# Optimization experiments

Measured on AMD Instinct MI355X. Metric: run time of the kernel, lower is better.

Reference implementation:

```python
import jax, jax.numpy as jnp
import numpy as np

GROUP_NORM_EPS = 1e-6
NUM_GROUPS = 32


def group_norm(x, gamma, beta, num_groups=NUM_GROUPS, eps=GROUP_NORM_EPS):
    B, H, W, C = x.shape
    g = num_groups
    xg = x.reshape(B, H, W, g, C // g)
    mean = jnp.mean(xg, axis=(1, 2, 4), keepdims=True)
    var = jnp.var(xg, axis=(1, 2, 4), keepdims=True)
    xn = ((xg - mean) * jax.lax.rsqrt(var + eps)).reshape(B, H, W, C)
    return xn * gamma + beta


def setup_inputs() -> dict:
    key = jax.random.key(0)
    ks = jax.random.split(key, 6)
    B, H, W, C = 4, 64, 64, 512
    scale = 1.0 / np.sqrt(C)
    return {
        "x": jax.random.normal(ks[0], (B, H, W, C), jnp.float32),
        "gn_gamma": jnp.ones((C,), jnp.float32),
        "gn_beta": jnp.zeros((C,), jnp.float32),
        "wq": jax.random.normal(ks[1], (C, C), jnp.float32) * scale,
        "bq": jnp.zeros((C,), jnp.float32),
        "wk": jax.random.normal(ks[2], (C, C), jnp.float32) * scale,
        "bk": jnp.zeros((C,), jnp.float32),
        "wv": jax.random.normal(ks[3], (C, C), jnp.float32) * scale,
        "bv": jnp.zeros((C,), jnp.float32),
        "wo": jax.random.normal(ks[4], (C, C), jnp.float32) * scale,
        "bo": jnp.zeros((C,), jnp.float32),
    }


def reference(x, gn_gamma, gn_beta, wq, bq, wk, bk, wv, bv, wo, bo):
    B, H, W, C = x.shape
    h = group_norm(x, gn_gamma, gn_beta)
    q = h @ wq + bq  # [B,H,W,C]
    k = h @ wk + bk
    v = h @ wv + bv
    N = H * W
    qf = q.reshape(B, N, C)
    kf = k.reshape(B, N, C)
    vf = v.reshape(B, N, C)
    # full spatial self-attention: [B, N, N] score matrix
    scores = jnp.einsum('bnc,bmc->bnm', qf, kf) * (C ** -0.5)
    attn = jax.nn.softmax(scores, axis=-1)
    out = jnp.einsum('bnm,bmc->bnc', attn, vf).reshape(B, H, W, C)
    out = out @ wo + bo
    return out + x
```

## Files before the change

### kernel.cpp

```cpp
#include <hip/hip_runtime.h>

typedef __bf16 bf16x8 __attribute__((ext_vector_type(8)));
typedef float  f32x4  __attribute__((ext_vector_type(4)));
typedef float  f32x16 __attribute__((ext_vector_type(16)));
typedef unsigned long long u64x2 __attribute__((ext_vector_type(2)));
typedef unsigned short u16;
typedef unsigned short us4 __attribute__((ext_vector_type(4)));

__device__ __forceinline__ u16 f2bf(float f) {
  __bf16 h = (__bf16)f;
  return __builtin_bit_cast(u16, h);
}

__device__ __forceinline__ void gload16(const void* g, void* l) {
  __builtin_amdgcn_global_load_lds(
      (const __attribute__((address_space(1))) unsigned int*)(g),
      (__attribute__((address_space(3))) unsigned int*)(l), 16, 0, 0);
}

__device__ __forceinline__ void barrier_lgkm() {
  asm volatile("s_waitcnt lgkmcnt(0)" ::: "memory");
  __builtin_amdgcn_s_barrier();
  asm volatile("" ::: "memory");
}
template <int N> __device__ __forceinline__ void vmwait() {
  asm volatile("s_waitcnt vmcnt(%0)" :: "n"(N) : "memory");
}

__global__ void gn_partial(const float* __restrict__ x, float* __restrict__ part) {
  const int chunk = blockIdx.x, g = blockIdx.y, b = blockIdx.z;
  const int tid = threadIdx.x;
  float s = 0.f, ss = 0.f;
  const float* xb = x + ((size_t)(b * 4096 + chunk * 512)) * 512 + g * 16;
  for (int i = tid; i < 2048; i += 256) {
    const int sp = i >> 2, c4 = (i & 3) << 2;
    const float4 v = *(const float4*)(xb + (size_t)sp * 512 + c4);
    s  += v.x + v.y + v.z + v.w;
    ss += v.x * v.x + v.y * v.y + v.z * v.z + v.w * v.w;
  }
  for (int m = 32; m; m >>= 1) { s += __shfl_xor(s, m); ss += __shfl_xor(ss, m); }
  __shared__ float red[8];
  const int w = tid >> 6;
  if ((tid & 63) == 0) { red[w * 2] = s; red[w * 2 + 1] = ss; }
  __syncthreads();
  if (tid == 0) {
    float S = 0.f, SS = 0.f;
    for (int i = 0; i < 4; ++i) { S += red[2 * i]; SS += red[2 * i + 1]; }
    const int idx = ((b * 32 + g) * 8 + chunk) * 2;
    part[idx] = S; part[idx + 1] = SS;
  }
}

__global__ void gn_finalize(const float* __restrict__ part, float* __restrict__ stats) {
  const int t = threadIdx.x;
  if (t < 128) {
    float S = 0.f, SS = 0.f;
    for (int i = 0; i < 8; ++i) { S += part[(t * 8 + i) * 2]; SS += part[(t * 8 + i) * 2 + 1]; }
    const float mean = S * (1.0f / 65536.0f);
    const float var  = SS * (1.0f / 65536.0f) - mean * mean;
    stats[t * 2] = mean;
    stats[t * 2 + 1] = rsqrtf(var + 1e-6f);
  }
}

__global__ void gn_apply(const float* __restrict__ x, const float* __restrict__ gamma,
                         const float* __restrict__ beta, const float* __restrict__ stats,
                         u16* __restrict__ h) {
  const size_t i = (size_t)blockIdx.x * 256 + threadIdx.x;
  const size_t e = i * 4;
  const int c = (int)(e & 511);
  const int b = (int)(e >> 21);
  const int g = c >> 4;
  const float mean = stats[(b * 32 + g) * 2];
  const float rstd = stats[(b * 32 + g) * 2 + 1];
  const float4 xv = *(const float4*)(x + e);
  const float4 gv = *(const float4*)(gamma + c);
  const float4 bv = *(const float4*)(beta + c);
  us4 hv;
  hv.x = f2bf((xv.x - mean) * rstd * gv.x + bv.x);
  hv.y = f2bf((xv.y - mean) * rstd * gv.y + bv.y);
  hv.z = f2bf((xv.z - mean) * rstd * gv.z + bv.z);
  hv.w = f2bf((xv.w - mean) * rstd * gv.w + bv.w);
  *(us4*)(h + e) = hv;
}

__global__ void wcast_t4(const float* __restrict__ wq, const float* __restrict__ wk,
                         const float* __restrict__ wv, const float* __restrict__ wo,
                         u16* __restrict__ wT) {
  const int idx = blockIdx.x * 256 + threadIdx.x;
  const int which = idx >> 18;
  const int rr = idx & 262143;
  const float* w = (which == 0) ? wq : (which == 1) ? wk : (which == 2) ? wv : wo;
  const int n = rr >> 9, k = rr & 511;
  wT[idx] = f2bf(w[k * 512 + n]);
}

#define GEMM_STAGE(buf, t)                                                       \
  {                                                                              \
    const int k0 = (t) * 32;                                                     \
    _Pragma("unroll")                                                            \
    for (int i = 0; i < 2; ++i) {                                                \
      const int cid = tid + i * 256;                                             \
      const int row = cid >> 2, cb = cid & 3;                                    \
      const int sc = (cb ^ (row & 3)) << 3;                                      \
      gload16(A + (size_t)(brow + row) * 512 + k0 + sc, &lA[buf][cid << 3]);     \
      gload16(Bt + (size_t)(bcol0 + row) * 512 + k0 + sc, &lB[buf][cid << 3]);   \
    }                                                                            \
  }

#define GEMM_MAIN                                                                \
  const f32x4 zero4 = {0.f, 0.f, 0.f, 0.f};                                      \
  f32x4 acc[4][4];                                                               \
  _Pragma("unroll") for (int a_ = 0; a_ < 4; ++a_)                               \
  _Pragma("unroll") for (int b_ = 0; b_ < 4; ++b_) acc[a_][b_] = zero4;          \
  GEMM_STAGE(0, 0);                                                              \
  asm volatile("s_waitcnt vmcnt(0)" ::: "memory");                               \
  __syncthreads();                                                               \
  int buf = 0;                                                                   \
  for (int t = 0; t < 16; ++t) {                                                 \
    if (t < 15) GEMM_STAGE(buf ^ 1, t + 1);                                      \
    bf16x8 af[4], bfv[4];                                                        \
    _Pragma("unroll") for (int f = 0; f < 4; ++f) {                              \
      const int ra = wr * 64 + f * 16 + l15;                                     \
      af[f] = *(const bf16x8*)(&lA[buf][(ra << 5) + ((lq ^ (ra & 3)) << 3)]);    \
      const int rb = wc * 64 + f * 16 + l15;                                     \
      bfv[f] = *(const bf16x8*)(&lB[buf][(rb << 5) + ((lq ^ (rb & 3)) << 3)]);   \
    }                                                                            \
    _Pragma("unroll") for (int fa = 0; fa < 4; ++fa)                             \
    _Pragma("unroll") for (int fb = 0; fb < 4; ++fb)                             \
      acc[fa][fb] = __builtin_amdgcn_mfma_f32_16x16x32_bf16(af[fa], bfv[fb],     \
                                                            acc[fa][fb], 0, 0, 0);\
    asm volatile("s_waitcnt vmcnt(0)" ::: "memory");                             \
    __syncthreads();                                                             \
    buf ^= 1;                                                                    \
  }

__global__ __launch_bounds__(256)
void gemm_oproj(const u16* __restrict__ A, const u16* __restrict__ Bt,
                const float* __restrict__ bias, const float* __restrict__ resid,
                float* __restrict__ Cout) {
  const int tid = threadIdx.x;
  const int wid = tid >> 6, l = tid & 63;
  const int wr = wid >> 1, wc = wid & 1;
  const int l15 = l & 15, lq = l >> 4;
  const int brow = blockIdx.x * 128, bcol0 = blockIdx.y * 128;
  __shared__ u16 lA[2][4096];
  __shared__ u16 lB[2][4096];
  GEMM_MAIN
#pragma unroll
  for (int fa = 0; fa < 4; ++fa)
#pragma unroll
    for (int fb = 0; fb < 4; ++fb) {
      const int col = bcol0 + wc * 64 + fb * 16 + l15;
      const float bv = bias[col];
#pragma unroll
      for (int i = 0; i < 4; ++i) {
        const int row = brow + wr * 64 + fa * 16 + lq * 4 + i;
        const size_t idx = (size_t)row * 512 + col;
        Cout[idx] = acc[fa][fb][i] + bv + resid[idx];
      }
    }
}

__global__ __launch_bounds__(256)
void gemm_qkv(const u16* __restrict__ A, const u16* __restrict__ wT,
              const float* __restrict__ bq, const float* __restrict__ bk,
              const float* __restrict__ bv_, u16* __restrict__ q,
              u16* __restrict__ k, u16* __restrict__ v8, float qs) {
  const int tid = threadIdx.x;
  const int wid = tid >> 6, l = tid & 63;
  const int wr = wid >> 1, wc = wid & 1;
  const int l15 = l & 15, lq = l >> 4;
  const int which = blockIdx.y >> 2;
  const int brow = blockIdx.x * 128, bcol0 = (blockIdx.y & 3) * 128;
  const u16* Bt = wT + which * 262144;
  const float* bias = (which == 0) ? bq : ((which == 1) ? bk : bv_);
  __shared__ u16 lA[2][4096];
  __shared__ u16 lB[2][4096];
  GEMM_MAIN
#pragma unroll
  for (int fa = 0; fa < 4; ++fa)
#pragma unroll
    for (int fb = 0; fb < 4; ++fb) {
      const int col = bcol0 + wc * 64 + fb * 16 + l15;
      const float bb_ = bias[col];
#pragma unroll
      for (int i = 0; i < 4; ++i) {
        const int row = brow + wr * 64 + fa * 16 + lq * 4 + i;
        const float v = acc[fa][fb][i] + bb_;
        if (which == 0) {
          q[(size_t)row * 512 + col] = f2bf(v * qs);
        } else if (which == 1) {
          k[(size_t)row * 512 + col] = f2bf(v);
        } else {
          const int bb = row >> 12, n = row & 4095;
          v8[((size_t)(bb * 512 + (n >> 3))) * 4096 +
             (size_t)((col ^ ((n >> 3) & 3)) << 3) + (n & 7)] = f2bf(v);
        }
      }
    }
}

__global__ __launch_bounds__(384)
void attn_kernel(const u16* __restrict__ Q, const u16* __restrict__ K,
                 const u16* __restrict__ V8, u16* __restrict__ Oo) {
  const int bid = blockIdx.x;
  const int b = bid & 3, qb = bid >> 2;
  const int tid = threadIdx.x;
  const int wid = tid >> 6, l = tid & 63;
  const int l31 = l & 31, lh = l >> 5;

  __shared__ __align__(16) char lds[75536];
  const int PB = 65536, AB = 74752, FL = 75264, LR = 75280;

  const u16* Kb = K + (size_t)b * 2097152;
  const u16* Vb = V8 + (size_t)b * 2097152;

  const f32x16 z16 = {0.f,0.f,0.f,0.f, 0.f,0.f,0.f,0.f, 0.f,0.f,0.f,0.f, 0.f,0.f,0.f,0.f};

  if (wid < 2) {
    const int qh = wid;
    bf16x8 qf[32];
    {
      const u16* qp = Q + ((size_t)(b * 4096 + qb * 64 + qh * 32 + l31)) * 512 + lh * 8;
#pragma unroll
      for (int kk = 0; kk < 32; ++kk) qf[kk] = *(const bf16x8*)(qp + kk * 16);
    }
    barrier_lgkm();
    float m_ = -3e38f, l_ = 0.f;
    const int kxor = (l31 & 15) << 4;
    for (int t = 0; t < 128; ++t) {
      const char* kb = lds + ((t & 1) << 15) + l31 * 1024;
      f32x16 a0 = z16, a1 = z16, a2 = z16, a3 = z16;
#pragma unroll
      for (int kk = 0; kk < 32; kk += 4) {
        const bf16x8 k0 = *(const bf16x8*)(kb + ((kk * 32 + lh * 16) ^ kxor));
        a0 = __builtin_amdgcn_mfma_f32_32x32x16_bf16(k0, qf[kk], a0, 0, 0, 0);
        const bf16x8 k1 = *(const bf16x8*)(kb + (((kk + 1) * 32 + lh * 16) ^ kxor));
        a1 = __builtin_amdgcn_mfma_f32_32x32x16_bf16(k1, qf[kk + 1], a1, 0, 0, 0);
        const bf16x8 k2 = *(const bf16x8*)(kb + (((kk + 2) * 32 + lh * 16) ^ kxor));
        a2 = __builtin_amdgcn_mfma_f32_32x32x16_bf16(k2, qf[kk + 2], a2, 0, 0, 0);
        const bf16x8 k3 = *(const bf16x8*)(kb + (((kk + 3) * 32 + lh * 16) ^ kxor));
        a3 = __builtin_amdgcn_mfma_f32_32x32x16_bf16(k3, qf[kk + 3], a3, 0, 0, 0);
      }
      const f32x16 s = (a0 + a1) + (a2 + a3);
      float tmax = fmaxf(s[0], s[1]);
#pragma unroll
      for (int r2 = 2; r2 < 16; ++r2) tmax = fmaxf(tmax, s[r2]);
      tmax = fmaxf(tmax, __shfl_xor(tmax, 32));
      const bool need = tmax > m_ + 8.0f;
      const float mn = need ? tmax : m_;
      const float al = need ? __expf(m_ - mn) : 1.0f;
      float p[16];
#pragma unroll
      for (int r2 = 0; r2 < 16; ++r2) p[r2] = __expf(s[r2] - mn);
      float ps = 0.f;
#pragma unroll
      for (int r2 = 0; r2 < 16; ++r2) ps += p[r2];
      ps += __shfl_xor(ps, 32);
      l_ = l_ * al + ps;
      m_ = mn;
      char* prow = lds + PB + (t & 1) * 4608 + (qh * 32 + l31) * 72;
#pragma unroll
      for (int rg = 0; rg < 4; ++rg) {
        us4 pk4;
        pk4.x = f2bf(p[rg * 4 + 0]); pk4.y = f2bf(p[rg * 4 + 1]);
        pk4.z = f2bf(p[rg * 4 + 2]); pk4.w = f2bf(p[rg * 4 + 3]);
        *(unsigned long long*)(prow + rg * 16 + lh * 8) =
            __builtin_bit_cast(unsigned long long, pk4);
      }
      if (lh == 0) *(float*)(lds + AB + (t & 1) * 256 + (qh * 32 + l31) * 4) = al;
      const bool anyn = __any(need);
      if (l == 0) *(int*)(lds + FL + ((t & 1) * 2 + qh) * 4) = anyn ? 1 : 0;
      barrier_lgkm();
    }
    if (lh == 0) *(float*)(lds + LR + (qh * 32 + l31) * 4) = l_;
    barrier_lgkm();
  } else {
    const int dq = wid - 2;
    const int stid = (wid - 2) * 64 + l;
    {
      char* kd = lds;
#pragma unroll
      for (int i = 0; i < 8; ++i) {
        const int cid = stid + i * 256;
        const int ob = cid << 4;
        const int n_ = ob >> 10;
        const int cb = (ob & 1023) ^ ((n_ & 15) << 4);
        gload16(Kb + (size_t)n_ * 512 + (cb >> 1), kd + ob);
      }
    }
    vmwait<0>();
    barrier_lgkm();
    f32x16 o[2][4];
#pragma unroll
    for (int qt = 0; qt < 2; ++qt)
#pragma unroll
      for (int f = 0; f < 4; ++f) o[qt][f] = z16;
    bf16x8 vrA[8], vrB[8];

#define PV_APPLY(PB_, VUSE)                                                      \
    {                                                                            \
      bf16x8 pa[2][2];                                                           \
      _Pragma("unroll") for (int qt = 0; qt < 2; ++qt)                           \
      _Pragma("unroll") for (int h2 = 0; h2 < 2; ++h2) {                         \
        const char* pr = lds + PB + (PB_) * 4608 + (qt * 32 + l31) * 72 +        \
                         h2 * 32 + lh * 16;                                      \
        u64x2 w2;                                                                \
        w2[0] = *(const unsigned long long*)pr;                                  \
        w2[1] = *(const unsigned long long*)(pr + 8);                            \
        pa[qt][h2] = __builtin_bit_cast(bf16x8, w2);                             \
      }                                                                          \
      const int fl = *(const int*)(lds + FL + (PB_) * 8) |                       \
                     *(const int*)(lds + FL + (PB_) * 8 + 4);                    \
      if (fl) {                                                                  \
        _Pragma("unroll") for (int qt = 0; qt < 2; ++qt)                         \
        _Pragma("unroll") for (int rg = 0; rg < 16; ++rg) {                      \
          const int cr = (rg & 3) + 8 * (rg >> 2) + 4 * lh;                      \
          const float av = *(const float*)(lds + AB + (PB_) * 256 +              \
                                           (qt * 32 + cr) * 4);                  \
          _Pragma("unroll") for (int f = 0; f < 4; ++f) o[qt][f][rg] *= av;      \
        }                                                                        \
      }                                                                          \
      _Pragma("unroll") for (int f = 0; f < 4; ++f)                              \
      _Pragma("unroll") for (int h2 = 0; h2 < 2; ++h2) {                         \
        o[0][f] = __builtin_amdgcn_mfma_f32_32x32x16_bf16(pa[0][h2],             \
                      VUSE[f * 2 + h2], o[0][f], 0, 0, 0);                       \
        o[1][f] = __builtin_amdgcn_mfma_f32_32x32x16_bf16(pa[1][h2],             \
                      VUSE[f * 2 + h2], o[1][f], 0, 0, 0);                       \
      }                                                                          \
    }

#define PV_STEP(T, VUSE, VLOAD)                                                  \
    {                                                                            \
      const int t_ = (T);                                                        \
      if (t_ < 127) {                                                            \
        const u16* ks = Kb + (size_t)(t_ + 1) * 16384;                           \
        char* kd = lds + (((t_ + 1) & 1) << 15);                                 \
        _Pragma("unroll") for (int i = 0; i < 8; ++i) {                          \
          const int cid = stid + i * 256;                                        \
          const int ob = cid << 4;                                               \
          const int n_ = ob >> 10;                                               \
          const int cb = (ob & 1023) ^ ((n_ & 15) << 4);                         \
          gload16(ks + (size_t)n_ * 512 + (cb >> 1), kd + ob);                   \
        }                                                                        \
      }                                                                          \
      vmwait<8>();                                       \
      if (t_ > 0) { PV_APPLY((t_ - 1) & 1, VUSE) }                               \
      {                                                                          \
        const u16* vsrc = Vb + (size_t)t_ * 16384;                               \
        _Pragma("unroll") for (int f = 0; f < 4; ++f)                            \
        _Pragma("unroll") for (int h2 = 0; h2 < 2; ++h2) {                       \
          const int c4 = h2 * 2 + lh;                                            \
          const int d = dq * 128 + f * 32 + l31;                                 \
          VLOAD[f * 2 + h2] =                                                    \
              *(const bf16x8*)(vsrc + ((size_t)(c4 * 512 + (d ^ c4)) << 3));     \
        }                                                                        \
      }                                                                          \
      vmwait<8>();                              \
      barrier_lgkm();                                                            \
    }

    for (int tt = 0; tt < 64; ++tt) {
      PV_STEP(2 * tt,     vrB, vrA)
      PV_STEP(2 * tt + 1, vrA, vrB)
    }
    vmwait<0>();
    PV_APPLY(1, vrB)
    barrier_lgkm();
#undef PV_STEP
#undef PV_APPLY
#pragma unroll
    for (int qt = 0; qt < 2; ++qt)
#pragma unroll
      for (int rg = 0; rg < 16; ++rg) {
        const int cr = (rg & 3) + 8 * (rg >> 2) + 4 * lh;
        const float li = 1.0f / *(const float*)(lds + LR + (qt * 32 + cr) * 4);
        u16* orow = Oo + ((size_t)(b * 4096 + qb * 64 + qt * 32 + cr)) * 512 + dq * 128 + l31;
#pragma unroll
        for (int f = 0; f < 4; ++f) orow[f * 32] = f2bf(o[qt][f][rg] * li);
      }
  }
}

extern "C" void kernel_launch(void* const* d_in, const int* in_sizes, int n_in,
                              void* d_out, int out_size, void* d_ws, size_t ws_size,
                              hipStream_t stream) {
  const float* x     = (const float*)d_in[0];
  const float* gamma = (const float*)d_in[1];
  const float* beta  = (const float*)d_in[2];
  const float* wq    = (const float*)d_in[3];
  const float* bq    = (const float*)d_in[4];
  const float* wk    = (const float*)d_in[5];
  const float* bk    = (const float*)d_in[6];
  const float* wv    = (const float*)d_in[7];
  const float* bv    = (const float*)d_in[8];
  const float* wo    = (const float*)d_in[9];
  const float* bo    = (const float*)d_in[10];
  float* out = (float*)d_out;

  char* ws = (char*)d_ws;
  const size_t SZ = (size_t)16384 * 512;
  u16* h    = (u16*)(ws);
  u16* q    = (u16*)(ws + SZ * 2);
  u16* k    = (u16*)(ws + SZ * 4);
  u16* v8   = (u16*)(ws + SZ * 6);
  u16* aout = (u16*)(ws + SZ * 8);
  u16* wT   = (u16*)(ws + SZ * 10);
  float* part  = (float*)(ws + SZ * 10 + 4 * 262144 * 2);
  float* stats = part + 2048;

  gn_partial<<<dim3(8, 32, 4), 256, 0, stream>>>(x, part);
  gn_finalize<<<1, 128, 0, stream>>>(part, stats);
  gn_apply<<<8192, 256, 0, stream>>>(x, gamma, beta, stats, h);

  wcast_t4<<<4096, 256, 0, stream>>>(wq, wk, wv, wo, wT);

  const float qs = 0.044194173824159216f;
  gemm_qkv<<<dim3(128, 12), 256, 0, stream>>>(h, wT, bq, bk, bv, q, k, v8, qs);

  attn_kernel<<<256, 384, 0, stream>>>(q, k, v8, aout);

  gemm_oproj<<<dim3(128, 4), 256, 0, stream>>>(aout, wT + 3 * 262144, bo, x, out);
}
```

Baseline: 265.6 us.

## Split attention KV range in two and merge halves with LSE combine kernel

The attention kernel now splits each batch's 4096 keys into two halves handled by separate blocks, doubling the grid from 256 to 512 blocks so all compute units get work. Each half writes a normalized partial output plus its log-sum-exp. A new combine kernel then reweights and merges the two partial outputs, reusing the h buffer as scratch for the second half. This adds an extra pass over the output and a small bf16 rounding step at the merge. The launch bounds hint is also raised to allow more resident blocks.

```diff
diff --git a/kernel.cpp b/kernel.cpp
--- a/kernel.cpp
+++ b/kernel.cpp
@@ -201,11 +201,12 @@
     }
 }
 
-__global__ __launch_bounds__(384)
+__global__ __launch_bounds__(384, 3)
 void attn_kernel(const u16* __restrict__ Q, const u16* __restrict__ K,
-                 const u16* __restrict__ V8, u16* __restrict__ Oo) {
+                 const u16* __restrict__ V8, u16* __restrict__ Op0,
+                 u16* __restrict__ Op1, float* __restrict__ lsep) {
   const int bid = blockIdx.x;
-  const int b = bid & 3, qb = bid >> 2;
+  const int b = bid & 3, z = (bid >> 2) & 1, qb = bid >> 3;
   const int tid = threadIdx.x;
   const int wid = tid >> 6, l = tid & 63;
   const int l31 = l & 31, lh = l >> 5;
@@ -213,8 +214,8 @@
   __shared__ __align__(16) char lds[75536];
   const int PB = 65536, AB = 74752, FL = 75264, LR = 75280;
 
-  const u16* Kb = K + (size_t)b * 2097152;
-  const u16* Vb = V8 + (size_t)b * 2097152;
+  const u16* Kb = K + (size_t)b * 2097152 + (size_t)z * 1048576;
+  const u16* Vb = V8 + (size_t)b * 2097152 + (size_t)z * 1048576;
 
   const f32x16 z16 = {0.f,0.f,0.f,0.f, 0.f,0.f,0.f,0.f, 0.f,0.f,0.f,0.f, 0.f,0.f,0.f,0.f};
 
@@ -229,7 +230,7 @@
     barrier_lgkm();
     float m_ = -3e38f, l_ = 0.f;
     const int kxor = (l31 & 15) << 4;
-    for (int t = 0; t < 128; ++t) {
+    for (int t = 0; t < 64; ++t) {
       const char* kb = lds + ((t & 1) << 15) + l31 * 1024;
       f32x16 a0 = z16, a1 = z16, a2 = z16, a3 = z16;
 #pragma unroll
@@ -274,7 +275,10 @@
       if (l == 0) *(int*)(lds + FL + ((t & 1) * 2 + qh) * 4) = anyn ? 1 : 0;
       barrier_lgkm();
     }
-    if (lh == 0) *(float*)(lds + LR + (qh * 32 + l31) * 4) = l_;
+    if (lh == 0) {
+      *(float*)(lds + LR + (qh * 32 + l31) * 4) = l_;
+      lsep[z * 16384 + b * 4096 + qb * 64 + qh * 32 + l31] = m_ + __logf(l_);
+    }
     barrier_lgkm();
   } else {
     const int dq = wid - 2;
@@ -334,7 +338,7 @@
 #define PV_STEP(T, VUSE, VLOAD)                                                  \
     {                                                                            \
       const int t_ = (T);                                                        \
-      if (t_ < 127) {                                                            \
+      if (t_ < 63) {                                                             \
         const u16* ks = Kb + (size_t)(t_ + 1) * 16384;                           \
         char* kd = lds + (((t_ + 1) & 1) << 15);                                 \
         _Pragma("unroll") for (int i = 0; i < 8; ++i) {                          \
@@ -361,7 +365,7 @@
       barrier_lgkm();                                                            \
     }
 
-    for (int tt = 0; tt < 64; ++tt) {
+    for (int tt = 0; tt < 32; ++tt) {
       PV_STEP(2 * tt,     vrB, vrA)
       PV_STEP(2 * tt + 1, vrA, vrB)
     }
@@ -370,17 +374,37 @@
     barrier_lgkm();
 #undef PV_STEP
 #undef PV_APPLY
+    u16* dstb = (z == 0 ? Op0 : Op1);
 #pragma unroll
     for (int qt = 0; qt < 2; ++qt)
 #pragma unroll
       for (int rg = 0; rg < 16; ++rg) {
         const int cr = (rg & 3) + 8 * (rg >> 2) + 4 * lh;
         const float li = 1.0f / *(const float*)(lds + LR + (qt * 32 + cr) * 4);
-        u16* orow = Oo + ((size_t)(b * 4096 + qb * 64 + qt * 32 + cr)) * 512 + dq * 128 + l31;
+        u16* orow = dstb + ((size_t)(b * 4096 + qb * 64 + qt * 32 + cr)) * 512 + dq * 128 + l31;
 #pragma unroll
         for (int f = 0; f < 4; ++f) orow[f * 32] = f2bf(o[qt][f][rg] * li);
       }
   }
+}
+
+__global__ void attn_combine(u16* __restrict__ O0, const u16* __restrict__ O1,
+                             const float* __restrict__ lsep) {
+  const int idx = blockIdx.x * 256 + threadIdx.x;
+  const int row = idx >> 6;
+  const int c8 = (idx & 63) << 3;
+  const float e0 = lsep[row], e1 = lsep[16384 + row];
+  const float M = fmaxf(e0, e1);
+  float w0 = __expf(e0 - M), w1 = __expf(e1 - M);
+  const float inv = 1.0f / (w0 + w1);
+  w0 *= inv; w1 *= inv;
+  const size_t base = (size_t)row * 512 + c8;
+  const bf16x8 a = *(const bf16x8*)(O0 + base);
+  const bf16x8 c = *(const bf16x8*)(O1 + base);
+  bf16x8 rr;
+#pragma unroll
+  for (int j = 0; j < 8; ++j) rr[j] = (__bf16)(w0 * (float)a[j] + w1 * (float)c[j]);
+  *(bf16x8*)(O0 + base) = rr;
 }
 
 extern "C" void kernel_launch(void* const* d_in, const int* in_sizes, int n_in,
@@ -409,6 +433,7 @@
   u16* wT   = (u16*)(ws + SZ * 10);
   float* part  = (float*)(ws + SZ * 10 + 4 * 262144 * 2);
   float* stats = part + 2048;
+  float* lse   = stats + 256;
 
   gn_partial<<<dim3(8, 32, 4), 256, 0, stream>>>(x, part);
   gn_finalize<<<1, 128, 0, stream>>>(part, stats);
@@ -419,7 +444,8 @@
   const float qs = 0.044194173824159216f;
   gemm_qkv<<<dim3(128, 12), 256, 0, stream>>>(h, wT, bq, bk, bv, q, k, v8, qs);
 
-  attn_kernel<<<256, 384, 0, stream>>>(q, k, v8, aout);
+  attn_kernel<<<512, 384, 0, stream>>>(q, k, v8, aout, h, lse);
+  attn_combine<<<4096, 256, 0, stream>>>(aout, h, lse);
 
   gemm_oproj<<<dim3(128, 4), 256, 0, stream>>>(aout, wT + 3 * 262144, bo, x, out);
 }
```

Result: slower. 953.0 us (+258.8%).

## Double warps in attention kernel and triple-buffer K tiles

Applied to the files above, without the earlier changes.

Raises the attention block from 6 to 12 waves. Four score waves now each handle 16 query rows using 16x16x32 MFMAs, and eight PV waves each own 64 output columns. K tiles move from double to triple buffering so loads are issued two tiles ahead. The aim is more in-flight work per CU and better hiding of K load latency, at the cost of more LDS per block (about 108KB) and possibly fewer resident blocks or register pressure under the new launch bounds.

```diff
diff --git a/kernel.cpp b/kernel.cpp
--- a/kernel.cpp
+++ b/kernel.cpp
@@ -3,7 +3,6 @@
 typedef __bf16 bf16x8 __attribute__((ext_vector_type(8)));
 typedef float  f32x4  __attribute__((ext_vector_type(4)));
 typedef float  f32x16 __attribute__((ext_vector_type(16)));
-typedef unsigned long long u64x2 __attribute__((ext_vector_type(2)));
 typedef unsigned short u16;
 typedef unsigned short us4 __attribute__((ext_vector_type(4)));
 
@@ -201,7 +200,7 @@
     }
 }
 
-__global__ __launch_bounds__(384)
+__global__ __launch_bounds__(768, 3)
 void attn_kernel(const u16* __restrict__ Q, const u16* __restrict__ K,
                  const u16* __restrict__ V8, u16* __restrict__ Oo) {
   const int bid = blockIdx.x;
@@ -209,155 +208,148 @@
   const int tid = threadIdx.x;
   const int wid = tid >> 6, l = tid & 63;
   const int l31 = l & 31, lh = l >> 5;
-
-  __shared__ __align__(16) char lds[75536];
-  const int PB = 65536, AB = 74752, FL = 75264, LR = 75280;
+  const int l15 = l & 15, lq = l >> 4;
+
+  __shared__ __align__(16) char lds[108320];
+  const int PB = 98304, AB = 107520, FL = 108032, LR = 108064;
 
   const u16* Kb = K + (size_t)b * 2097152;
   const u16* Vb = V8 + (size_t)b * 2097152;
 
-  const f32x16 z16 = {0.f,0.f,0.f,0.f, 0.f,0.f,0.f,0.f, 0.f,0.f,0.f,0.f, 0.f,0.f,0.f,0.f};
-
-  if (wid < 2) {
-    const int qh = wid;
-    bf16x8 qf[32];
+  const f32x4 z4 = {0.f, 0.f, 0.f, 0.f};
+
+  if (wid < 4) {
+    const int w = wid;
+    bf16x8 qf[16];
     {
-      const u16* qp = Q + ((size_t)(b * 4096 + qb * 64 + qh * 32 + l31)) * 512 + lh * 8;
-#pragma unroll
-      for (int kk = 0; kk < 32; ++kk) qf[kk] = *(const bf16x8*)(qp + kk * 16);
+      const u16* qp = Q + ((size_t)(b * 4096 + qb * 64 + w * 16 + l15)) * 512 + lq * 8;
+#pragma unroll
+      for (int kk = 0; kk < 16; ++kk) qf[kk] = *(const bf16x8*)(qp + kk * 32);
     }
     barrier_lgkm();
     float m_ = -3e38f, l_ = 0.f;
-    const int kxor = (l31 & 15) << 4;
+    const int swz = l15 << 4;
     for (int t = 0; t < 128; ++t) {
-      const char* kb = lds + ((t & 1) << 15) + l31 * 1024;
-      f32x16 a0 = z16, a1 = z16, a2 = z16, a3 = z16;
-#pragma unroll
-      for (int kk = 0; kk < 32; kk += 4) {
-        const bf16x8 k0 = *(const bf16x8*)(kb + ((kk * 32 + lh * 16) ^ kxor));
-        a0 = __builtin_amdgcn_mfma_f32_32x32x16_bf16(k0, qf[kk], a0, 0, 0, 0);
-        const bf16x8 k1 = *(const bf16x8*)(kb + (((kk + 1) * 32 + lh * 16) ^ kxor));
-        a1 = __builtin_amdgcn_mfma_f32_32x32x16_bf16(k1, qf[kk + 1], a1, 0, 0, 0);
-        const bf16x8 k2 = *(const bf16x8*)(kb + (((kk + 2) * 32 + lh * 16) ^ kxor));
-        a2 = __builtin_amdgcn_mfma_f32_32x32x16_bf16(k2, qf[kk + 2], a2, 0, 0, 0);
-        const bf16x8 k3 = *(const bf16x8*)(kb + (((kk + 3) * 32 + lh * 16) ^ kxor));
-        a3 = __builtin_amdgcn_mfma_f32_32x32x16_bf16(k3, qf[kk + 3], a3, 0, 0, 0);
+      const char* kb = lds + (t % 3) * 32768;
+      const char* r0 = kb + l15 * 1024;
+      const char* r1 = kb + (16 + l15) * 1024;
+      f32x4 a0 = z4, a1 = z4, a2 = z4, a3 = z4;
+#pragma unroll
+      for (int kk = 0; kk < 16; kk += 2) {
+        const int o0 = (kk * 64 + lq * 16) ^ swz;
+        const int o1 = ((kk + 1) * 64 + lq * 16) ^ swz;
+        a0 = __builtin_amdgcn_mfma_f32_16x16x32_bf16(*(const bf16x8*)(r0 + o0), qf[kk], a0, 0, 0, 0);
+        a1 = __builtin_amdgcn_mfma_f32_16x16x32_bf16(*(const bf16x8*)(r1 + o0), qf[kk], a1, 0, 0, 0);
+        a2 = __builtin_amdgcn_mfma_f32_16x16x32_bf16(*(const bf16x8*)(r0 + o1), qf[kk + 1], a2, 0, 0, 0);
+        a3 = __builtin_amdgcn_mfma_f32_16x16x32_bf16(*(const bf16x8*)(r1 + o1), qf[kk + 1], a3, 0, 0, 0);
       }
-      const f32x16 s = (a0 + a1) + (a2 + a3);
-      float tmax = fmaxf(s[0], s[1]);
-#pragma unroll
-      for (int r2 = 2; r2 < 16; ++r2) tmax = fmaxf(tmax, s[r2]);
+      const f32x4 s0 = a0 + a2;
+      const f32x4 s1 = a1 + a3;
+      float tmax = fmaxf(fmaxf(fmaxf(s0[0], s0[1]), fmaxf(s0[2], s0[3])),
+                         fmaxf(fmaxf(s1[0], s1[1]), fmaxf(s1[2], s1[3])));
+      tmax = fmaxf(tmax, __shfl_xor(tmax, 16));
       tmax = fmaxf(tmax, __shfl_xor(tmax, 32));
       const bool need = tmax > m_ + 8.0f;
       const float mn = need ? tmax : m_;
       const float al = need ? __expf(m_ - mn) : 1.0f;
-      float p[16];
-#pragma unroll
-      for (int r2 = 0; r2 < 16; ++r2) p[r2] = __expf(s[r2] - mn);
-      float ps = 0.f;
-#pragma unroll
-      for (int r2 = 0; r2 < 16; ++r2) ps += p[r2];
+      float p0[4], p1[4];
+#pragma unroll
+      for (int i = 0; i < 4; ++i) { p0[i] = __expf(s0[i] - mn); p1[i] = __expf(s1[i] - mn); }
+      float ps = (p0[0] + p0[1]) + (p0[2] + p0[3]) + (p1[0] + p1[1]) + (p1[2] + p1[3]);
+      ps += __shfl_xor(ps, 16);
       ps += __shfl_xor(ps, 32);
       l_ = l_ * al + ps;
       m_ = mn;
-      char* prow = lds + PB + (t & 1) * 4608 + (qh * 32 + l31) * 72;
-#pragma unroll
-      for (int rg = 0; rg < 4; ++rg) {
-        us4 pk4;
-        pk4.x = f2bf(p[rg * 4 + 0]); pk4.y = f2bf(p[rg * 4 + 1]);
-        pk4.z = f2bf(p[rg * 4 + 2]); pk4.w = f2bf(p[rg * 4 + 3]);
-        *(unsigned long long*)(prow + rg * 16 + lh * 8) =
-            __builtin_bit_cast(unsigned long long, pk4);
-      }
-      if (lh == 0) *(float*)(lds + AB + (t & 1) * 256 + (qh * 32 + l31) * 4) = al;
+      char* prow = lds + PB + (t & 1) * 4608 + (w * 16 + l15) * 72;
+      us4 k0, k1;
+      k0.x = f2bf(p0[0]); k0.y = f2bf(p0[1]); k0.z = f2bf(p0[2]); k0.w = f2bf(p0[3]);
+      k1.x = f2bf(p1[0]); k1.y = f2bf(p1[1]); k1.z = f2bf(p1[2]); k1.w = f2bf(p1[3]);
+      *(unsigned long long*)(prow + lq * 8)      = __builtin_bit_cast(unsigned long long, k0);
+      *(unsigned long long*)(prow + 32 + lq * 8) = __builtin_bit_cast(unsigned long long, k1);
+      if (lq == 0) *(float*)(lds + AB + (t & 1) * 256 + (w * 16 + l15) * 4) = al;
       const bool anyn = __any(need);
-      if (l == 0) *(int*)(lds + FL + ((t & 1) * 2 + qh) * 4) = anyn ? 1 : 0;
+      if (l == 0) *(int*)(lds + FL + (t & 1) * 16 + w * 4) = anyn ? 1 : 0;
       barrier_lgkm();
     }
-    if (lh == 0) *(float*)(lds + LR + (qh * 32 + l31) * 4) = l_;
+    if (lq == 0) *(float*)(lds + LR + (w * 16 + l15) * 4) = l_;
     barrier_lgkm();
   } else {
-    const int dq = wid - 2;
-    const int stid = (wid - 2) * 64 + l;
-    {
-      char* kd = lds;
-#pragma unroll
-      for (int i = 0; i < 8; ++i) {
-        const int cid = stid + i * 256;
-        const int ob = cid << 4;
-        const int n_ = ob >> 10;
-        const int cb = (ob & 1023) ^ ((n_ & 15) << 4);
-        gload16(Kb + (size_t)n_ * 512 + (cb >> 1), kd + ob);
-      }
-    }
-    vmwait<0>();
+    const int pw = wid - 4;
+    const int dbase = pw * 64;
+    const int stid = pw * 64 + l;
+
+#define STAGEK(TT)                                                     \
+    {                                                                  \
+      const u16* ks = Kb + (size_t)(TT) * 16384;                       \
+      char* kd = lds + ((TT) % 3) * 32768;                             \
+      _Pragma("unroll") for (int i = 0; i < 4; ++i) {                  \
+        const int cid = stid + i * 512;                                \
+        const int ob = cid << 4;                                       \
+        const int n_ = ob >> 10;                                       \
+        const int cb = (ob & 1023) ^ ((n_ & 15) << 4);                 \
+        gload16(ks + (size_t)n_ * 512 + (cb >> 1), kd + ob);           \
+      }                                                                \
+    }
+
+    STAGEK(0)
+    STAGEK(1)
+    vmwait<4>();
     barrier_lgkm();
-    f32x16 o[2][4];
+    f32x16 oA[2][2];
+    const f32x16 z16 = {0.f,0.f,0.f,0.f, 0.f,0.f,0.f,0.f, 0.f,0.f,0.f,0.f, 0.f,0.f,0.f,0.f};
 #pragma unroll
     for (int qt = 0; qt < 2; ++qt)
 #pragma unroll
-      for (int f = 0; f < 4; ++f) o[qt][f] = z16;
-    bf16x8 vrA[8], vrB[8];
+      for (int dt = 0; dt < 2; ++dt) oA[qt][dt] = z16;
+    bf16x8 vrA[4], vrB[4];
 
 #define PV_APPLY(PB_, VUSE)                                                      \
     {                                                                            \
       bf16x8 pa[2][2];                                                           \
       _Pragma("unroll") for (int qt = 0; qt < 2; ++qt)                           \
-      _Pragma("unroll") for (int h2 = 0; h2 < 2; ++h2) {                         \
+      _Pragma("unroll") for (int kh = 0; kh < 2; ++kh) {                         \
         const char* pr = lds + PB + (PB_) * 4608 + (qt * 32 + l31) * 72 +        \
-                         h2 * 32 + lh * 16;                                      \
-        u64x2 w2;                                                                \
+                         kh * 32 + lh * 16;                                      \
+        unsigned long long w2[2];                                                \
         w2[0] = *(const unsigned long long*)pr;                                  \
         w2[1] = *(const unsigned long long*)(pr + 8);                            \
-        pa[qt][h2] = __builtin_bit_cast(bf16x8, w2);                             \
+        pa[qt][kh] = __builtin_bit_cast(bf16x8, w2);                             \
       }                                                                          \
-      const int fl = *(const int*)(lds + FL + (PB_) * 8) |                       \
-                     *(const int*)(lds + FL + (PB_) * 8 + 4);                    \
+      const int* flp = (const int*)(lds + FL + (PB_) * 16);                      \
+      const int fl = flp[0] | flp[1] | flp[2] | flp[3];                          \
       if (fl) {                                                                  \
         _Pragma("unroll") for (int qt = 0; qt < 2; ++qt)                         \
         _Pragma("unroll") for (int rg = 0; rg < 16; ++rg) {                      \
           const int cr = (rg & 3) + 8 * (rg >> 2) + 4 * lh;                      \
           const float av = *(const float*)(lds + AB + (PB_) * 256 +              \
                                            (qt * 32 + cr) * 4);                  \
-          _Pragma("unroll") for (int f = 0; f < 4; ++f) o[qt][f][rg] *= av;      \
+          oA[qt][0][rg] *= av; oA[qt][1][rg] *= av;                              \
         }                                                                        \
       }                                                                          \
-      _Pragma("unroll") for (int f = 0; f < 4; ++f)                              \
-      _Pragma("unroll") for (int h2 = 0; h2 < 2; ++h2) {                         \
-        o[0][f] = __builtin_amdgcn_mfma_f32_32x32x16_bf16(pa[0][h2],             \
-                      VUSE[f * 2 + h2], o[0][f], 0, 0, 0);                       \
-        o[1][f] = __builtin_amdgcn_mfma_f32_32x32x16_bf16(pa[1][h2],             \
-                      VUSE[f * 2 + h2], o[1][f], 0, 0, 0);                       \
-      }                                                                          \
+      _Pragma("unroll") for (int qt = 0; qt < 2; ++qt)                           \
+      _Pragma("unroll") for (int dt = 0; dt < 2; ++dt)                           \
+      _Pragma("unroll") for (int kh = 0; kh < 2; ++kh)                           \
+        oA[qt][dt] = __builtin_amdgcn_mfma_f32_32x32x16_bf16(pa[qt][kh],         \
+                        VUSE[dt * 2 + kh], oA[qt][dt], 0, 0, 0);                 \
     }
 
 #define PV_STEP(T, VUSE, VLOAD)                                                  \
     {                                                                            \
       const int t_ = (T);                                                        \
-      if (t_ < 127) {                                                            \
-        const u16* ks = Kb + (size_t)(t_ + 1) * 16384;                           \
-        char* kd = lds + (((t_ + 1) & 1) << 15);                                 \
-        _Pragma("unroll") for (int i = 0; i < 8; ++i) {                          \
-          const int cid = stid + i * 256;                                        \
-          const int ob = cid << 4;                                               \
-          const int n_ = ob >> 10;                                               \
-          const int cb = (ob & 1023) ^ ((n_ & 15) << 4);                         \
-          gload16(ks + (size_t)n_ * 512 + (cb >> 1), kd + ob);                   \
-        }                                                                        \
-      }                                                                          \
-      vmwait<8>();                                       \
+      if (t_ < 126) STAGEK(t_ + 2)                                               \
+      vmwait<4>();                                   \
       if (t_ > 0) { PV_APPLY((t_ - 1) & 1, VUSE) }                               \
       {                                                                          \
         const u16* vsrc = Vb + (size_t)t_ * 16384;                               \
-        _Pragma("unroll") for (int f = 0; f < 4; ++f)                            \
-        _Pragma("unroll") for (int h2 = 0; h2 < 2; ++h2) {                       \
-          const int c4 = h2 * 2 + lh;                                            \
-          const int d = dq * 128 + f * 32 + l31;                                 \
-          VLOAD[f * 2 + h2] =                                                    \
+        _Pragma("unroll") for (int dt = 0; dt < 2; ++dt)                         \
+        _Pragma("unroll") for (int kh = 0; kh < 2; ++kh) {                       \
+          const int c4 = kh * 2 + lh;                                            \
+          const int d = dbase + dt * 32 + l31;                                   \
+          VLOAD[dt * 2 + kh] =                                                   \
               *(const bf16x8*)(vsrc + ((size_t)(c4 * 512 + (d ^ c4)) << 3));     \
         }                                                                        \
       }                                                                          \
-      vmwait<8>();                              \
+      vmwait<8>();                               \
       barrier_lgkm();                                                            \
     }
 
@@ -370,15 +362,16 @@
     barrier_lgkm();
 #undef PV_STEP
 #undef PV_APPLY
+#undef STAGEK
 #pragma unroll
     for (int qt = 0; qt < 2; ++qt)
 #pragma unroll
       for (int rg = 0; rg < 16; ++rg) {
         const int cr = (rg & 3) + 8 * (rg >> 2) + 4 * lh;
         const float li = 1.0f / *(const float*)(lds + LR + (qt * 32 + cr) * 4);
-        u16* orow = Oo + ((size_t)(b * 4096 + qb * 64 + qt * 32 + cr)) * 512 + dq * 128 + l31;
-#pragma unroll
-        for (int f = 0; f < 4; ++f) orow[f * 32] = f2bf(o[qt][f][rg] * li);
+        u16* orow = Oo + ((size_t)(b * 4096 + qb * 64 + qt * 32 + cr)) * 512 + dbase + l31;
+        orow[0]  = f2bf(oA[qt][0][rg] * li);
+        orow[32] = f2bf(oA[qt][1][rg] * li);
       }
   }
 }
@@ -419,7 +412,7 @@
   const float qs = 0.044194173824159216f;
   gemm_qkv<<<dim3(128, 12), 256, 0, stream>>>(h, wT, bq, bk, bv, q, k, v8, qs);
 
-  attn_kernel<<<256, 384, 0, stream>>>(q, k, v8, aout);
+  attn_kernel<<<256, 768, 0, stream>>>(q, k, v8, aout);
 
   gemm_oproj<<<dim3(128, 4), 256, 0, stream>>>(aout, wT + 3 * 262144, bo, x, out);
 }
```

Measured after the change: 250.0 us. 5.9% less time.
